# Optimization experiments

Hardware: AMD Instinct MI355X
Metric: run time of the kernel (lower is better)

The kernel has to match this reference:

```python
import jax, jax.numpy as jnp
import numpy as np
from jax import lax

C_DIM = 64
N_HEADS = 8
PATCH = 3
PAD = (PATCH - 1) // 2
EPS = 1e-6


def _unfold(x, p, pad):
    # x: [B,C,H,W] -> [B, C*p*p, H*W], torch.F.unfold ordering (C slowest, then ph, pw)
    B, C, H, W = x.shape
    xp = jnp.pad(x, ((0, 0), (0, 0), (pad, pad), (pad, pad)))
    cols = jnp.stack([xp[:, :, i:i + H, j:j + W] for i in range(p) for j in range(p)], axis=2)
    return cols.reshape(B, C * p * p, H * W)


def _fold(cols, p, pad, H, W):
    # cols: [B, C*p*p, H*W] -> [B,C,H,W] via col2im scatter-add (torch.F.fold)
    B = cols.shape[0]
    C = cols.shape[1] // (p * p)
    cols = cols.reshape(B, C, p * p, H, W)
    out = jnp.zeros((B, C, H + 2 * pad, W + 2 * pad), cols.dtype)
    for i in range(p):
        for j in range(p):
            out = out.at[:, :, i:i + H, j:j + W].add(cols[:, :, i * p + j])
    return out[:, :, pad:pad + H, pad:pad + W]


def _linear_attn(q, k, v):
    # q,k,v: [B, h, N, d]; non-softmax linear attention with ReLU features
    kv = jnp.einsum('bhnd,bhne->bhde', k, v)          # [B,h,d,d]
    ksum = k.sum(axis=2)                              # [B,h,d]
    denom = jnp.einsum('bhnd,bhd->bhn', q, ksum) + EPS
    out = jnp.einsum('bhnd,bhde->bhne', q, kv) / denom[..., None]
    return out


def setup_inputs() -> dict:
    key = jax.random.key(0)
    ks = jax.random.split(key, 5)
    B, C, H, W = 4, C_DIM, 128, 128
    x = jax.random.normal(ks[0], (B, C, H, W), jnp.float32)
    w_qkv = jax.random.normal(ks[1], (3 * C, C), jnp.float32) * 0.05
    b_qkv = jax.random.normal(ks[2], (3 * C,), jnp.float32) * 0.01
    w_proj = jax.random.normal(ks[3], (C, C, 3, 3), jnp.float32) * 0.05
    b_proj = jax.random.normal(ks[4], (C,), jnp.float32) * 0.01
    return {"x": x, "w_qkv": w_qkv, "b_qkv": b_qkv, "w_proj": w_proj, "b_proj": b_proj}


def reference(x, w_qkv, b_qkv, w_proj, b_proj):
    B, C, H, W = x.shape
    p, pad, h = PATCH, PAD, N_HEADS
    N = H * W
    # 1x1 conv qkv
    qkv = jnp.einsum('bchw,oc->bohw', x, w_qkv) + b_qkv[None, :, None, None]
    q, k, v = qkv[:, :C], qkv[:, C:2 * C], qkv[:, 2 * C:]
    q = jax.nn.relu(q)
    k = jax.nn.relu(k)
    # im2col: [B, C*p*p, N]
    qc = _unfold(q, p, pad)
    kc = _unfold(k, p, pad)
    vc = _unfold(v, p, pad)
    d = (C * p * p) // h
    qh = qc.reshape(B, h, d, N).transpose(0, 1, 3, 2)  # [B,h,N,d]
    kh = kc.reshape(B, h, d, N).transpose(0, 1, 3, 2)
    vh = vc.reshape(B, h, d, N).transpose(0, 1, 3, 2)
    o = _linear_attn(qh, kh, vh)                       # [B,h,N,d]
    oc = o.transpose(0, 1, 3, 2).reshape(B, C * p * p, N)
    folded = _fold(oc, p, pad, H, W)
    ones_cols = _unfold(jnp.ones((B, C, H, W), x.dtype), p, pad)
    counts = _fold(ones_cols, p, pad, H, W)
    y = folded / counts
    # 3x3 proj conv
    y = lax.conv_general_dilated(y, w_proj, (1, 1), [(1, 1), (1, 1)],
                                 dimension_numbers=('NCHW', 'OIHW', 'NCHW'))
    y = y + b_proj[None, :, None, None]
    return y
```

## Files before the change

kernel.cpp:

```cpp
#include <hip/hip_runtime.h>

#define BB 4
#define CC 64
#define HH 128
#define WW 128
#define NN (HH*WW)
#define HP 130
#define NPP (HP*HP)
#define HPS 136
#define VROWS 132
#define NPPS (VROWS*HPS)
#define HP2 132
#define NPP2 (HP2*HP2)
#define NH 8
#define DD 72

__global__ __launch_bounds__(256) void kz_pads(float* __restrict__ Qp, float* __restrict__ Kp,
                                               float* __restrict__ rfp){
    const int t = threadIdx.x;
    const int c = blockIdx.x;
    if (c < 256){
        float* f = Qp + (size_t)c*NPP2;
        for (int idx=t; idx<4*HP2; idx+=256){
            int rs = idx / HP2, col = idx - rs*HP2;
            int row = (rs<2)? rs : (128+rs);
            f[row*HP2 + col] = 0.f;
        }
        for (int idx=t; idx<128*4; idx+=256){
            int row = 2 + (idx>>2), cs = idx&3;
            int col = (cs<2)? cs : (128+cs);
            f[row*HP2 + col] = 0.f;
        }
    } else if (c < 768){
        float* f = Kp + (size_t)(c-256)*NPPS;
        for (int idx=t; idx<4*HPS; idx+=256){
            int rs = idx / HPS, col = idx - rs*HPS;
            int row = (rs<2)? rs : (128+rs);
            f[row*HPS + col] = 0.f;
        }
        for (int idx=t; idx<128*8; idx+=256){
            int row = 2 + (idx>>3), cs = idx&7;
            int col = (cs<4)? cs : (128+cs);
            f[row*HPS + col] = 0.f;
        }
    } else {
        float* f = rfp + (size_t)(c-768)*NPP;
        for (int idx=t; idx<2*HP; idx+=256){
            int rs = idx / HP, col = idx - rs*HP;
            f[(rs?129:0)*HP + col] = 0.f;
        }
        for (int idx=t; idx<128*2; idx+=256){
            int row = 1 + (idx>>1);
            f[row*HP + ((idx&1)?129:0)] = 0.f;
        }
    }
}

__global__ __launch_bounds__(256) void k0_wt(const float* __restrict__ wproj,
                                             const float* __restrict__ wqkv,
                                             float* __restrict__ wt, float* __restrict__ wqkvT){
    int idx = blockIdx.x*256 + threadIdx.x;
    if (idx < 64*9*64){
        int oc = idx & 63;
        int w  = (idx >> 6) % 9;
        int ci = idx / 576;
        wt[idx] = wproj[(oc*64 + ci)*9 + w];
    } else if (idx < 64*9*64 + 3*64*64){
        int i2 = idx - 64*9*64;
        int orel = i2 & 63, c = (i2 >> 6) & 63, gy = i2 >> 12;
        wqkvT[i2] = wqkv[(gy*64 + orel)*64 + c];
    }
}

__global__ __launch_bounds__(256) void k1_qkv(const float* __restrict__ x,
        const float* __restrict__ wqkvT, const float* __restrict__ bqkv,
        float* __restrict__ Qp, float* __restrict__ Kp, float* __restrict__ Vp){
    const int t = threadIdx.x;
    const int gy = blockIdx.y;
    const int b  = blockIdx.z;
    const int pix = blockIdx.x*256 + t;
    float acc[64];
#pragma unroll
    for (int o=0;o<64;++o) acc[o]=0.f;
    const float* xb = x + (size_t)(b*64)*NN + pix;
    const float* wT = wqkvT + gy*4096;
    for (int c=0;c<64;++c){
        float xv = xb[(size_t)c*NN];
        const float4* wr = (const float4*)(wT + c*64);
#pragma unroll
        for (int o4=0;o4<16;++o4){
            float4 wv = wr[o4];
            acc[o4*4+0] += xv*wv.x;
            acc[o4*4+1] += xv*wv.y;
            acc[o4*4+2] += xv*wv.z;
            acc[o4*4+3] += xv*wv.w;
        }
    }
    const int y = pix >> 7, xx = pix & 127;
    float* dst; size_t cstride;
    if (gy == 0){ dst = Qp + (size_t)(b*64)*NPP2 + (y+2)*HP2 + (xx+2); cstride = NPP2; }
    else { dst = ((gy==1)?Kp:Vp) + (size_t)(b*64)*NPPS + (y+2)*HPS + (xx+4); cstride = NPPS; }
    const bool dorelu = (gy < 2);
    const float* bl = bqkv + gy*64;
#pragma unroll
    for (int o=0;o<64;++o){
        float v = acc[o] + bl[o];
        if (dorelu) v = fmaxf(v, 0.f);
        dst[(size_t)o*cstride] = v;
    }
}

__global__ __launch_bounds__(256) void k2_ksum(const float* __restrict__ Kp, float* __restrict__ ksum){
    const int c = blockIdx.x, b = blockIdx.y;
    const float* src = Kp + (size_t)(b*64 + c)*NPPS;
    float a[3][3];
#pragma unroll
    for (int i=0;i<3;++i)
#pragma unroll
        for (int j=0;j<3;++j) a[i][j]=0.f;
    for (int idx = threadIdx.x; idx < NPPS; idx += 256){
        int r = idx / HPS, cc = idx - r*HPS;
        float v = src[idx];
#pragma unroll
        for (int i=0;i<3;++i){
            bool fy = (unsigned)(r - 1 - i) < 128u;
#pragma unroll
            for (int j=0;j<3;++j){
                bool fx = (unsigned)(cc - 3 - j) < 128u;
                if (fy && fx) a[i][j] += v;
            }
        }
    }
    __shared__ float red[4][9];
#pragma unroll
    for (int i=0;i<3;++i)
#pragma unroll
        for (int j=0;j<3;++j){
            float v = a[i][j];
            for (int m=1;m<64;m<<=1) v += __shfl_xor(v, m, 64);
            a[i][j] = v;
        }
    int wave = threadIdx.x >> 6, lane = threadIdx.x & 63;
    if (lane == 0){
#pragma unroll
        for (int w=0;w<9;++w) red[wave][w] = a[w/3][w%3];
    }
    __syncthreads();
    if (threadIdx.x < 9){
        float s = red[0][threadIdx.x]+red[1][threadIdx.x]+red[2][threadIdx.x]+red[3][threadIdx.x];
        int h = c >> 3, cl = c & 7;
        ksum[(b*NH + h)*DD + cl*9 + threadIdx.x] = s;
    }
}

__global__ __launch_bounds__(256) void k3a_corr(const float* __restrict__ Kp, const float* __restrict__ Vp,
                                                float* __restrict__ Cpart){
    const int t = threadIdx.x;
    const int pair = blockIdx.x;
    const int cd = pair >> 3, ce = pair & 7;
    const int h = blockIdx.y, b = blockIdx.z;
    const int bh = b*NH + h;
    const float* Kc = Kp + (size_t)(b*64 + h*8 + cd)*NPPS;
    const float* Vc = Vp + (size_t)(b*64 + h*8 + ce)*NPPS;
    const int x0 = (t & 31) * 4;
    const int yb = t >> 5;
    const int y0 = yb*16;
    float C[25];
#pragma unroll
    for (int k=0;k<25;++k) C[k]=0.f;

    float vv[5][12];
    const float* vbase = Vc + (size_t)y0*HPS + x0;
#pragma unroll
    for (int rr=0; rr<4; ++rr){
#pragma unroll
        for (int q=0;q<3;++q){
            float4 a = *(const float4*)(vbase + rr*HPS + 4*q);
            vv[rr][4*q]=a.x; vv[rr][4*q+1]=a.y; vv[rr][4*q+2]=a.z; vv[rr][4*q+3]=a.w;
        }
    }
#pragma unroll
    for (int it=0; it<16; ++it){
        const int slot = (it+4)%5;
#pragma unroll
        for (int q=0;q<3;++q){
            float4 a = *(const float4*)(vbase + (it+4)*HPS + 4*q);
            vv[slot][4*q]=a.x; vv[slot][4*q+1]=a.y; vv[slot][4*q+2]=a.z; vv[slot][4*q+3]=a.w;
        }
        float4 kk4 = *(const float4*)(Kc + (size_t)(y0+it+2)*HPS + 4 + x0);
        float kk[4] = {kk4.x, kk4.y, kk4.z, kk4.w};
#pragma unroll
        for (int dr=0; dr<5; ++dr){
            const float* vrow = vv[(it+dr)%5];
#pragma unroll
            for (int dj=0; dj<5; ++dj)
#pragma unroll
                for (int p=0; p<4; ++p)
                    C[dr*5+dj] += kk[p] * vrow[p+dj+2];
        }
    }
#pragma unroll
    for (int k=0;k<25;++k){
        float v = C[k];
        for (int m=1;m<64;m<<=1) v += __shfl_xor(v, m, 64);
        C[k] = v;
    }
    __shared__ float red[4][25];
    const int wave = t >> 6, lane = t & 63;
    if (lane == 0){
#pragma unroll
        for (int k=0;k<25;++k) red[wave][k] = C[k];
    }
    __syncthreads();
    if (t < 25){
        float s = red[0][t]+red[1][t]+red[2][t]+red[3][t];
        Cpart[((size_t)bh*64 + pair)*25 + t] = s;
    }
}

__global__ __launch_bounds__(128) void k3c_kv(const float* __restrict__ Kp, const float* __restrict__ Vp,
                                              const float* __restrict__ Cpart, float* __restrict__ kvT2){
    __shared__ float Krow[2][136];
    __shared__ float Vrow[10][136];
    __shared__ float Kcol[132][2];
    __shared__ float Vcol[132][16];
    __shared__ float corr[100];
    __shared__ float C25s[25];
    const int t = threadIdx.x;
    const int pair = blockIdx.x;
    const int cd = pair >> 3, ce = pair & 7;
    const int h = blockIdx.y, b = blockIdx.z;
    const int bh = b*NH + h;
    const float* Kc = Kp + (size_t)(b*64 + h*8 + cd)*NPPS;
    const float* Vc = Vp + (size_t)(b*64 + h*8 + ce)*NPPS;
    for (int idx=t; idx<2*136; idx+=128){
        int side = idx/136, col = idx - side*136;
        Krow[side][col] = Kc[(side?129:2)*HPS + col];
    }
    for (int idx=t; idx<10*136; idx+=128){
        int s = idx/136, col = idx - s*136;
        int row = (s<5)? s : (122+s);
        Vrow[s][col] = Vc[row*HPS + col];
    }
    for (int idx=t; idx<132*2; idx+=128){
        int row = idx>>1, side = idx&1;
        Kcol[row][side] = Kc[row*HPS + (side?131:4)];
    }
    for (int idx=t; idx<132*16; idx+=128){
        int row = idx>>4, g = idx&15;
        Vcol[row][g] = Vc[row*HPS + ((g<8)? g : (120+g))];
    }
    __syncthreads();
    if (t < 100){
        int kind = t/50, rem = t%50, side = rem/25, sh = rem%25;
        int di2 = sh/5, dj2 = sh - di2*5;
        float s = 0.f;
        if (kind == 0){
            const float* kr = &Krow[side][4];
            const float* vr = &Vrow[side*5+di2][2+dj2];
            for (int bb=0; bb<128; ++bb) s += kr[bb]*vr[bb];
        } else {
            const int g = side? (9+dj2) : (2+dj2);
            for (int a=0; a<128; ++a) s += Kcol[2+a][side]*Vcol[a+di2][g];
        }
        corr[t] = s;
    } else if (t < 125){
        C25s[t-100] = Cpart[((size_t)bh*64 + pair)*25 + (t-100)];
    }
    __syncthreads();
    if (t < 81){
        int i = t/27, j = (t/9)%3, i2 = (t/3)%3, j2 = t%3;
        int di2 = i2-i+2, dj2 = j2-j+2;
        float val = C25s[di2*5+dj2];
        int si = (i==0)?1:0;
        int sj = (j==0)?1:0;
        if (i != 1) val -= corr[si*25 + di2*5 + dj2];
        if (j != 1) val -= corr[50 + sj*25 + di2*5 + dj2];
        if (i != 1 && j != 1){
            int cj = (j==0)?127:0;
            val += Krow[si][4+cj] * Vrow[si*5+di2][2+cj+dj2];
        }
        kvT2[((size_t)bh*DD + ce*9 + i2*3 + j2)*96 + cd*12 + i*3 + j] = val;
    }
}

__global__ __launch_bounds__(256) void k4_r(const float* __restrict__ Qp, const float* __restrict__ ksum,
                                            float* __restrict__ rfp){
    const int h = blockIdx.y, b = blockIdx.z;
    __shared__ float ks[72];
    if (threadIdx.x < 72) ks[threadIdx.x] = ksum[(b*NH + h)*DD + threadIdx.x];
    __syncthreads();
    const int pix = blockIdx.x*256 + threadIdx.x;
    const int y = pix >> 7, xx = pix & 127;
    const float* Qb = Qp + (size_t)(b*64 + h*8)*NPP2 + (y+1)*HP2 + (xx+1);
    float denom = 0.f;
#pragma unroll
    for (int cl=0; cl<8; ++cl){
        const float* q = Qb + (size_t)cl*NPP2;
#pragma unroll
        for (int w=0; w<9; ++w){
            denom += q[(w/3)*HP2 + (w%3)] * ks[cl*9 + w];
        }
    }
    rfp[(size_t)(b*NH + h)*NPP + (y+1)*HP + (xx+1)] = 1.f/(denom + 1e-6f);
}

__global__ __launch_bounds__(512) void k5_attn(const float* __restrict__ Qp, const float* __restrict__ kvT2,
          const float* __restrict__ rfp, float* __restrict__ folded){
    __shared__ __align__(16) float Qt[8*20*20];
    __shared__ __align__(16) float rt[18*20];
    const int t = threadIdx.x;
    const int tile = blockIdx.x;
    const int h = blockIdx.y, b = blockIdx.z;
    const int ty0 = (tile >> 3)*16, tx0 = (tile & 7)*16;

    const float* Qb = Qp + (size_t)(b*64 + h*8)*NPP2 + (size_t)ty0*HP2 + tx0;
    for (int idx=t; idx<8*20*20; idx+=512){
        int cl = idx / 400; int rem = idx - cl*400; int r = rem/20, cc = rem - r*20;
        Qt[idx] = Qb[(size_t)cl*NPP2 + r*HP2 + cc];
    }
    const float* rg = rfp + (size_t)(b*NH + h)*NPP + (size_t)ty0*HP + tx0;
    for (int idx=t; idx<18*18; idx+=512){
        int rr = idx / 18, cc = idx - rr*18;
        rt[rr*20 + cc] = rg[rr*HP + cc];
    }
    __syncthreads();

    const int c  = __builtin_amdgcn_readfirstlane(t >> 6);
    const int l  = t & 63;
    const int pr = l >> 2;
    const int pc = (l & 3) * 4;

    const float* kvc = kvT2 + ((size_t)(b*NH + h)*DD + c*9)*96;

    float acc[9][4];
#pragma unroll
    for (int u=0;u<9;++u)
#pragma unroll
        for (int p=0;p<4;++p) acc[u][p]=0.f;

    for (int cl=0; cl<8; ++cl){
        float qw[5][8];
        const float* qb = &Qt[cl*400 + pr*20 + pc];
#pragma unroll
        for (int rr=0; rr<5; ++rr){
            float4 a0 = *(const float4*)(qb + rr*20);
            float4 a1 = *(const float4*)(qb + rr*20 + 4);
            qw[rr][0]=a0.x; qw[rr][1]=a0.y; qw[rr][2]=a0.z; qw[rr][3]=a0.w;
            qw[rr][4]=a1.x; qw[rr][5]=a1.y; qw[rr][6]=a1.z; qw[rr][7]=a1.w;
        }
#pragma unroll
        for (int u=0; u<9; ++u){
            const float* kr = kvc + u*96 + cl*12;
            float kw[9];
#pragma unroll
            for (int i=0;i<9;++i) kw[i] = kr[i];
            const int iu = u/3, ju = u - iu*3;
#pragma unroll
            for (int w=0; w<9; ++w){
                const int rr = (w/3) - iu + 2;
                const int cc = (w%3) - ju + 2;
#pragma unroll
                for (int p=0;p<4;++p)
                    acc[u][p] += qw[rr][cc+p] * kw[w];
            }
        }
    }
    float rw[3][6];
    const float* rb = &rt[pr*20 + pc];
#pragma unroll
    for (int rr=0; rr<3; ++rr)
#pragma unroll
        for (int j=0; j<6; ++j) rw[rr][j] = rb[rr*20 + j];
    float out[4];
#pragma unroll
    for (int p=0;p<4;++p) out[p]=0.f;
#pragma unroll
    for (int u=0; u<9; ++u){
        const int iu = u/3, ju = u - iu*3;
#pragma unroll
        for (int p=0;p<4;++p)
            out[p] += acc[u][p] * rw[2-iu][p+2-ju];
    }
    const int iy = ty0 + pr;
    const float ry = 3.f - (float)(iy==0) - (float)(iy==127);
#pragma unroll
    for (int p=0;p<4;++p){
        const int ix = tx0 + pc + p;
        const float rx = 3.f - (float)(ix==0) - (float)(ix==127);
        out[p] = out[p] / (ry*rx);
    }
    float4 o4 = make_float4(out[0], out[1], out[2], out[3]);
    *(float4*)(&folded[(size_t)(b*64 + h*8 + c)*NN + (ty0+pr)*WW + tx0 + pc]) = o4;
}

__global__ __launch_bounds__(256) void k6_conv(const float* __restrict__ folded, const float* __restrict__ wt,
         const float* __restrict__ bproj, float* __restrict__ out){
    __shared__ float ut[64*120];
    const int t = threadIdx.x;
    const int tile = blockIdx.x;
    const int b = blockIdx.y;
    const int ty0 = (tile >> 4)*8, tx0 = (tile & 15)*8;

    for (int idx=t; idx<6400; idx+=256){
        int ci = idx / 100; int rem = idx - ci*100; int rr = rem/10, cc = rem - rr*10;
        int iy = ty0 - 1 + rr, ix = tx0 - 1 + cc;
        float v = 0.f;
        if ((unsigned)iy < 128u && (unsigned)ix < 128u)
            v = folded[(size_t)(b*64 + ci)*NN + iy*WW + ix];
        ut[ci*120 + rr*12 + cc] = v;
    }
    __syncthreads();

    const int wv4 = __builtin_amdgcn_readfirstlane(t >> 6);
    const int ocb = wv4*16;
    const int l  = t & 63;
    const int pr = l >> 3, pc = l & 7;

    float acc[16];
#pragma unroll
    for (int o=0;o<16;++o) acc[o]=0.f;

    const float* ub0 = &ut[pr*12 + pc];
    const float* wb  = wt + ocb;
    for (int ci=0; ci<64; ++ci){
        float u[9];
        const float* uc = ub0 + ci*120;
#pragma unroll
        for (int dy=0;dy<3;++dy)
#pragma unroll
            for (int dx=0;dx<3;++dx) u[dy*3+dx] = uc[dy*12 + dx];
#pragma unroll
        for (int w=0;w<9;++w){
            const float* kr = wb + (ci*9 + w)*64;
            const float uv = u[w];
#pragma unroll
            for (int o=0;o<16;++o) acc[o] += kr[o]*uv;
        }
    }
    const int y = ty0 + pr, x = tx0 + pc;
    const float* bb = bproj + ocb;
    float* dst = &out[(size_t)(b*64 + ocb)*NN + y*WW + x];
#pragma unroll
    for (int o=0;o<16;++o) dst[(size_t)o*NN] = acc[o] + bb[o];
}

extern "C" void kernel_launch(void* const* d_in, const int* in_sizes, int n_in,
                              void* d_out, int out_size, void* d_ws, size_t ws_size,
                              hipStream_t stream) {
    const float* x     = (const float*)d_in[0];
    const float* wqkv  = (const float*)d_in[1];
    const float* bqkv  = (const float*)d_in[2];
    const float* wproj = (const float*)d_in[3];
    const float* bproj = (const float*)d_in[4];
    float* out = (float*)d_out;
    float* ws  = (float*)d_ws;

    const size_t szQ2 = (size_t)BB*CC*NPP2;
    const size_t szFS = (size_t)BB*CC*NPPS;
    const size_t szR  = (size_t)BB*NH*NPP;
    const size_t szKV = (size_t)BB*NH*DD*96;
    const size_t szKS = (size_t)BB*NH*DD;
    float* Qp2    = ws;
    float* Kp     = Qp2 + szQ2;
    float* Vp     = Kp + szFS;
    float* rfp    = Vp + szFS;
    float* kvT2   = rfp + szR;
    float* ksum   = kvT2 + szKV;
    float* folded = ksum + szKS;
    float* wt     = folded + (size_t)BB*CC*NN;
    float* wqkvT  = wt + (size_t)64*9*64;
    float* Cpart  = folded;

    kz_pads <<<dim3(800),      256, 0, stream>>>(Qp2, Kp, rfp);
    k0_wt   <<<dim3(192),      256, 0, stream>>>(wproj, wqkv, wt, wqkvT);
    k1_qkv  <<<dim3(64, 3, 4), 256, 0, stream>>>(x, wqkvT, bqkv, Qp2, Kp, Vp);
    k2_ksum <<<dim3(64, 4),    256, 0, stream>>>(Kp, ksum);
    k3a_corr<<<dim3(64, 8, 4), 256, 0, stream>>>(Kp, Vp, Cpart);
    k3c_kv  <<<dim3(64, 8, 4), 128, 0, stream>>>(Kp, Vp, Cpart, kvT2);
    k4_r    <<<dim3(64, 8, 4), 256, 0, stream>>>(Qp2, ksum, rfp);
    k5_attn <<<dim3(64, 8, 4), 512, 0, stream>>>(Qp2, kvT2, rfp, folded);
    k6_conv <<<dim3(256, 4),   256, 0, stream>>>(folded, wt, bproj, out);
}
```

Measured before the change: 345.4 us.

## Fuse denominator computation into attention kernel and interleave conv smem channels

Drops the separate k4_r kernel and the padded rfp buffer. Each attention block now computes the reciprocal denominators for its 18x18 halo tile from the Q tile already in shared memory, with out-of-image positions set to zero. This removes one launch and a global write and read of the denominator map, at the cost of recomputing halo values in each tile. The conv kernel's shared-memory layout also interleaves channel pairs, with row stride 24, which is meant to cut LDS bank conflicts.

```diff
diff --git a/kernel.cpp b/kernel.cpp
--- a/kernel.cpp
+++ b/kernel.cpp
@@ -5,8 +5,6 @@
 #define HH 128
 #define WW 128
 #define NN (HH*WW)
-#define HP 130
-#define NPP (HP*HP)
 #define HPS 136
 #define VROWS 132
 #define NPPS (VROWS*HPS)
@@ -15,8 +13,7 @@
 #define NH 8
 #define DD 72
 
-__global__ __launch_bounds__(256) void kz_pads(float* __restrict__ Qp, float* __restrict__ Kp,
-                                               float* __restrict__ rfp){
+__global__ __launch_bounds__(256) void kz_pads(float* __restrict__ Qp, float* __restrict__ Kp){
     const int t = threadIdx.x;
     const int c = blockIdx.x;
     if (c < 256){
@@ -31,7 +28,7 @@
             int col = (cs<2)? cs : (128+cs);
             f[row*HP2 + col] = 0.f;
         }
-    } else if (c < 768){
+    } else {
         float* f = Kp + (size_t)(c-256)*NPPS;
         for (int idx=t; idx<4*HPS; idx+=256){
             int rs = idx / HPS, col = idx - rs*HPS;
@@ -42,16 +39,6 @@
             int row = 2 + (idx>>3), cs = idx&7;
             int col = (cs<4)? cs : (128+cs);
             f[row*HPS + col] = 0.f;
-        }
-    } else {
-        float* f = rfp + (size_t)(c-768)*NPP;
-        for (int idx=t; idx<2*HP; idx+=256){
-            int rs = idx / HP, col = idx - rs*HP;
-            f[(rs?129:0)*HP + col] = 0.f;
-        }
-        for (int idx=t; idx<128*2; idx+=256){
-            int row = 1 + (idx>>1);
-            f[row*HP + ((idx&1)?129:0)] = 0.f;
         }
     }
 }
@@ -284,45 +271,41 @@
     }
 }
 
-__global__ __launch_bounds__(256) void k4_r(const float* __restrict__ Qp, const float* __restrict__ ksum,
-                                            float* __restrict__ rfp){
-    const int h = blockIdx.y, b = blockIdx.z;
-    __shared__ float ks[72];
-    if (threadIdx.x < 72) ks[threadIdx.x] = ksum[(b*NH + h)*DD + threadIdx.x];
-    __syncthreads();
-    const int pix = blockIdx.x*256 + threadIdx.x;
-    const int y = pix >> 7, xx = pix & 127;
-    const float* Qb = Qp + (size_t)(b*64 + h*8)*NPP2 + (y+1)*HP2 + (xx+1);
-    float denom = 0.f;
-#pragma unroll
-    for (int cl=0; cl<8; ++cl){
-        const float* q = Qb + (size_t)cl*NPP2;
-#pragma unroll
-        for (int w=0; w<9; ++w){
-            denom += q[(w/3)*HP2 + (w%3)] * ks[cl*9 + w];
-        }
-    }
-    rfp[(size_t)(b*NH + h)*NPP + (y+1)*HP + (xx+1)] = 1.f/(denom + 1e-6f);
-}
-
 __global__ __launch_bounds__(512) void k5_attn(const float* __restrict__ Qp, const float* __restrict__ kvT2,
-          const float* __restrict__ rfp, float* __restrict__ folded){
+          const float* __restrict__ ksum, float* __restrict__ folded){
     __shared__ __align__(16) float Qt[8*20*20];
     __shared__ __align__(16) float rt[18*20];
+    __shared__ float ks[72];
     const int t = threadIdx.x;
     const int tile = blockIdx.x;
     const int h = blockIdx.y, b = blockIdx.z;
     const int ty0 = (tile >> 3)*16, tx0 = (tile & 7)*16;
+    const int bh = b*NH + h;
 
     const float* Qb = Qp + (size_t)(b*64 + h*8)*NPP2 + (size_t)ty0*HP2 + tx0;
     for (int idx=t; idx<8*20*20; idx+=512){
         int cl = idx / 400; int rem = idx - cl*400; int r = rem/20, cc = rem - r*20;
         Qt[idx] = Qb[(size_t)cl*NPP2 + r*HP2 + cc];
     }
-    const float* rg = rfp + (size_t)(b*NH + h)*NPP + (size_t)ty0*HP + tx0;
-    for (int idx=t; idx<18*18; idx+=512){
-        int rr = idx / 18, cc = idx - rr*18;
-        rt[rr*20 + cc] = rg[rr*HP + cc];
+    if (t < 72) ks[t] = ksum[(size_t)bh*DD + t];
+    __syncthreads();
+
+    if (t < 324){
+        int rr = t/18, cc = t - rr*18;
+        int py = ty0 - 1 + rr, px = tx0 - 1 + cc;
+        float rv = 0.f;
+        if ((unsigned)py < 128u && (unsigned)px < 128u){
+            float denom = 0.f;
+#pragma unroll
+            for (int cl=0; cl<8; ++cl){
+                const float* qb2 = &Qt[cl*400 + rr*20 + cc];
+#pragma unroll
+                for (int w=0; w<9; ++w)
+                    denom += qb2[(w/3)*20 + (w%3)] * ks[cl*9 + w];
+            }
+            rv = 1.f/(denom + 1e-6f);
+        }
+        rt[rr*20 + cc] = rv;
     }
     __syncthreads();
 
@@ -331,7 +314,7 @@
     const int pr = l >> 2;
     const int pc = (l & 3) * 4;
 
-    const float* kvc = kvT2 + ((size_t)(b*NH + h)*DD + c*9)*96;
+    const float* kvc = kvT2 + ((size_t)bh*DD + c*9)*96;
 
     float acc[9][4];
 #pragma unroll
@@ -341,11 +324,11 @@
 
     for (int cl=0; cl<8; ++cl){
         float qw[5][8];
-        const float* qb = &Qt[cl*400 + pr*20 + pc];
+        const float* qb2 = &Qt[cl*400 + pr*20 + pc];
 #pragma unroll
         for (int rr=0; rr<5; ++rr){
-            float4 a0 = *(const float4*)(qb + rr*20);
-            float4 a1 = *(const float4*)(qb + rr*20 + 4);
+            float4 a0 = *(const float4*)(qb2 + rr*20);
+            float4 a1 = *(const float4*)(qb2 + rr*20 + 4);
             qw[rr][0]=a0.x; qw[rr][1]=a0.y; qw[rr][2]=a0.z; qw[rr][3]=a0.w;
             qw[rr][4]=a1.x; qw[rr][5]=a1.y; qw[rr][6]=a1.z; qw[rr][7]=a1.w;
         }
@@ -396,7 +379,7 @@
 
 __global__ __launch_bounds__(256) void k6_conv(const float* __restrict__ folded, const float* __restrict__ wt,
          const float* __restrict__ bproj, float* __restrict__ out){
-    __shared__ float ut[64*120];
+    __shared__ float ut[32*240];
     const int t = threadIdx.x;
     const int tile = blockIdx.x;
     const int b = blockIdx.y;
@@ -408,7 +391,7 @@
         float v = 0.f;
         if ((unsigned)iy < 128u && (unsigned)ix < 128u)
             v = folded[(size_t)(b*64 + ci)*NN + iy*WW + ix];
-        ut[ci*120 + rr*12 + cc] = v;
+        ut[(ci>>1)*240 + rr*24 + (ci&1)*12 + cc] = v;
     }
     __syncthreads();
 
@@ -421,15 +404,14 @@
 #pragma unroll
     for (int o=0;o<16;++o) acc[o]=0.f;
 
-    const float* ub0 = &ut[pr*12 + pc];
     const float* wb  = wt + ocb;
     for (int ci=0; ci<64; ++ci){
         float u[9];
-        const float* uc = ub0 + ci*120;
+        const float* uc = &ut[(ci>>1)*240 + (ci&1)*12 + pr*24 + pc];
 #pragma unroll
         for (int dy=0;dy<3;++dy)
 #pragma unroll
-            for (int dx=0;dx<3;++dx) u[dy*3+dx] = uc[dy*12 + dx];
+            for (int dx=0;dx<3;++dx) u[dy*3+dx] = uc[dy*24 + dx];
 #pragma unroll
         for (int w=0;w<9;++w){
             const float* kr = wb + (ci*9 + w)*64;
@@ -458,27 +440,24 @@
 
     const size_t szQ2 = (size_t)BB*CC*NPP2;
     const size_t szFS = (size_t)BB*CC*NPPS;
-    const size_t szR  = (size_t)BB*NH*NPP;
     const size_t szKV = (size_t)BB*NH*DD*96;
     const size_t szKS = (size_t)BB*NH*DD;
     float* Qp2    = ws;
     float* Kp     = Qp2 + szQ2;
     float* Vp     = Kp + szFS;
-    float* rfp    = Vp + szFS;
-    float* kvT2   = rfp + szR;
+    float* kvT2   = Vp + szFS;
     float* ksum   = kvT2 + szKV;
     float* folded = ksum + szKS;
     float* wt     = folded + (size_t)BB*CC*NN;
     float* wqkvT  = wt + (size_t)64*9*64;
     float* Cpart  = folded;
 
-    kz_pads <<<dim3(800),      256, 0, stream>>>(Qp2, Kp, rfp);
+    kz_pads <<<dim3(768),      256, 0, stream>>>(Qp2, Kp);
     k0_wt   <<<dim3(192),      256, 0, stream>>>(wproj, wqkv, wt, wqkvT);
     k1_qkv  <<<dim3(64, 3, 4), 256, 0, stream>>>(x, wqkvT, bqkv, Qp2, Kp, Vp);
     k2_ksum <<<dim3(64, 4),    256, 0, stream>>>(Kp, ksum);
     k3a_corr<<<dim3(64, 8, 4), 256, 0, stream>>>(Kp, Vp, Cpart);
     k3c_kv  <<<dim3(64, 8, 4), 128, 0, stream>>>(Kp, Vp, Cpart, kvT2);
-    k4_r    <<<dim3(64, 8, 4), 256, 0, stream>>>(Qp2, ksum, rfp);
-    k5_attn <<<dim3(64, 8, 4), 512, 0, stream>>>(Qp2, kvT2, rfp, folded);
+    k5_attn <<<dim3(64, 8, 4), 512, 0, stream>>>(Qp2, kvT2, ksum, folded);
     k6_conv <<<dim3(256, 4),   256, 0, stream>>>(folded, wt, bproj, out);
 }
```

Result: no change. 344.2 us (-0.3%).
